# Kernel tuning notes

Measured on AMD Instinct MI355X. Metric: run time of the kernel, lower is better.

The kernel has to match this reference:

```python
import jax, jax.numpy as jnp
import numpy as np

N_NODES = 4096
N_EDGES = 16384
F_IN = 64
F_EDGE = 16
HID = 128
OUT = 64
N_GRAPHS = 32


def _encoder(x, edge_index, edge_attr, batch, p):
    N = x.shape[0]
    src, dst = edge_index[0], edge_index[1]
    # EdgeMLP: [E, F_edge] -> [E, F_in * HID] per-edge weight matrices
    h = jax.nn.relu(edge_attr @ p['e_w1'] + p['e_b1'])
    h = jax.nn.relu(h @ p['e_w2'] + p['e_b2'])
    Wmat = (h @ p['e_w3'] + p['e_b3']).reshape(-1, x.shape[1], p['root_w'].shape[1])  # [E, F_in, HID]
    # NNConv: message = x_src @ W_edge, scatter-add to dst, plus root transform + bias
    msg = jnp.einsum('ei,eio->eo', x[src], Wmat)  # [E, HID]
    agg = jax.ops.segment_sum(msg, dst, num_segments=N)
    h1 = jax.nn.relu(agg + x @ p['root_w'] + p['conv1_b'])  # [N, HID]
    # GATConv (1 head, concat=False) with self-loops (PyG default)
    loop = jnp.arange(N, dtype=src.dtype)
    si = jnp.concatenate([src, loop])
    di = jnp.concatenate([dst, loop])
    hp = h1 @ p['gat_w']  # [N, HID]
    a_s = hp @ p['att_src']  # [N]
    a_d = hp @ p['att_dst']  # [N]
    e = jax.nn.leaky_relu(a_s[si] + a_d[di], negative_slope=0.2)
    m = jax.ops.segment_max(e, di, num_segments=N)
    ex = jnp.exp(e - m[di])
    denom = jax.ops.segment_sum(ex, di, num_segments=N)
    alpha = ex / (denom[di] + 1e-16)
    h2 = jax.ops.segment_sum(alpha[:, None] * hp[si], di, num_segments=N) + p['gat_b']
    h2 = jax.nn.relu(h2)
    # global mean pool over graphs
    s = jax.ops.segment_sum(h2, batch, num_segments=N_GRAPHS)
    cnt = jax.ops.segment_sum(jnp.ones((N,), h2.dtype), batch, num_segments=N_GRAPHS)
    pooled = s / jnp.maximum(cnt, 1.0)[:, None]
    return jax.nn.relu(pooled @ p['fc1_w'] + p['fc1_b'])  # [B, OUT]


def setup_inputs() -> dict:
    key = jax.random.key(0)
    ks = jax.random.split(key, 24)
    d = {}
    d['x1'] = jax.random.normal(ks[0], (N_NODES, F_IN), jnp.float32)
    d['edge_index1'] = jax.random.randint(ks[1], (2, N_EDGES), 0, N_NODES)
    d['edge_attr1'] = jax.random.normal(ks[2], (N_EDGES, F_EDGE), jnp.float32)
    d['batch1'] = jnp.sort(jax.random.randint(ks[3], (N_NODES,), 0, N_GRAPHS))
    d['x2'] = jax.random.normal(ks[4], (N_NODES, F_IN), jnp.float32)
    d['edge_index2'] = jax.random.randint(ks[5], (2, N_EDGES), 0, N_NODES)
    d['edge_attr2'] = jax.random.normal(ks[6], (N_EDGES, F_EDGE), jnp.float32)
    d['batch2'] = jnp.sort(jax.random.randint(ks[7], (N_NODES,), 0, N_GRAPHS))

    def lin(k, fi, fo):
        return jax.random.normal(k, (fi, fo), jnp.float32) * (fi ** -0.5)

    d['e_w1'] = lin(ks[8], F_EDGE, 128); d['e_b1'] = jnp.zeros((128,), jnp.float32)
    d['e_w2'] = lin(ks[9], 128, 64); d['e_b2'] = jnp.zeros((64,), jnp.float32)
    d['e_w3'] = lin(ks[10], 64, F_IN * HID); d['e_b3'] = jnp.zeros((F_IN * HID,), jnp.float32)
    d['root_w'] = lin(ks[11], F_IN, HID); d['conv1_b'] = jnp.zeros((HID,), jnp.float32)
    d['gat_w'] = lin(ks[12], HID, HID)
    d['att_src'] = jax.random.normal(ks[13], (HID,), jnp.float32) * (HID ** -0.5)
    d['att_dst'] = jax.random.normal(ks[14], (HID,), jnp.float32) * (HID ** -0.5)
    d['gat_b'] = jnp.zeros((HID,), jnp.float32)
    d['fc1_w'] = lin(ks[15], HID, OUT); d['fc1_b'] = jnp.zeros((OUT,), jnp.float32)
    d['fc2_w'] = lin(ks[16], OUT, 1); d['fc2_b'] = jnp.zeros((1,), jnp.float32)
    return d


def reference(x1, edge_index1, edge_attr1, batch1, x2, edge_index2, edge_attr2, batch2,
              e_w1, e_b1, e_w2, e_b2, e_w3, e_b3, root_w, conv1_b,
              gat_w, att_src, att_dst, gat_b, fc1_w, fc1_b, fc2_w, fc2_b):
    p = dict(e_w1=e_w1, e_b1=e_b1, e_w2=e_w2, e_b2=e_b2, e_w3=e_w3, e_b3=e_b3,
             root_w=root_w, conv1_b=conv1_b, gat_w=gat_w, att_src=att_src,
             att_dst=att_dst, gat_b=gat_b, fc1_w=fc1_w, fc1_b=fc1_b,
             fc2_w=fc2_w, fc2_b=fc2_b)
    z1 = _encoder(x1, edge_index1, edge_attr1, batch1, p)
    z2 = _encoder(x2, edge_index2, edge_attr2, batch2, p)
    z = jnp.abs(z1 - z2) @ fc2_w + fc2_b  # [B, 1]
    return jax.nn.sigmoid(z).squeeze(1)  # [B]
```

## Files before the change

kernel.cpp:

```cpp
#include <hip/hip_runtime.h>
#include <hip/hip_bf16.h>
#include <math.h>

#define NN 4096
#define NE 16384
#define FIN 64
#define FE 16
#define HIDD 128
#define OUTD 64
#define NG 32
#define EP (NE + NN)
#define KSPLIT 2
#define NCH (64 / KSPLIT)

typedef __attribute__((ext_vector_type(4))) unsigned u4v;
typedef __attribute__((ext_vector_type(4))) float f4v;
typedef _Float16 f16x8 __attribute__((ext_vector_type(8)));

union FragH { u4v u; f16x8 h; };
union FH2 { _Float16 f[2]; unsigned u; };
union F16x8U { _Float16 f[8]; u4v u; };

#define PB_EMLP  4096
#define PB_BIAS  (PB_EMLP + 4096)
#define PB_HIST  (PB_BIAS + 32)
#define PB_TOTAL (PB_HIST + 64)

__global__ void k_prep(const float* __restrict__ ea0, const float* __restrict__ ea1,
                       const float* __restrict__ w1, const float* __restrict__ b1,
                       const float* __restrict__ w2, const float* __restrict__ b2,
                       const float* __restrict__ w3,
                       const float* __restrict__ X0, const float* __restrict__ X1,
                       const float* __restrict__ b3,
                       const int* __restrict__ ei0, const int* __restrict__ ei1,
                       unsigned short* __restrict__ B1t,
                       float* __restrict__ h0, float* __restrict__ h1g,
                       float* __restrict__ Bb0, float* __restrict__ Bb1,
                       int* __restrict__ rowcnt) {
    int b = blockIdx.x, t = threadIdx.x;
    if (b < PB_EMLP) {
        int gi = b >> 11;
        int e0 = (b & 2047) * 8;
        const float* ea = gi ? ea1 : ea0;
        float* hout = gi ? h1g : h0;
        __shared__ float h1s[8][HIDD];
#pragma unroll
        for (int r = 0; r < 4; ++r) {
            int idx = r * 256 + t;
            int e1 = idx >> 7, j = idx & 127;
            float acc = b1[j];
#pragma unroll
            for (int i = 0; i < FE; ++i) acc += ea[(e0 + e1) * FE + i] * w1[i * HIDD + j];
            h1s[e1][j] = fmaxf(acc, 0.f);
        }
        __syncthreads();
#pragma unroll
        for (int r = 0; r < 2; ++r) {
            int idx = r * 256 + t;
            int e1 = idx >> 6, j = idx & 63;
            float acc = b2[j];
#pragma unroll 16
            for (int k = 0; k < HIDD; ++k) acc += h1s[e1][k] * w2[k * 64 + j];
            hout[(size_t)(e0 + e1) * 64 + j] = fmaxf(acc, 0.f);
        }
    } else if (b < PB_BIAS) {
        int bb = b - PB_EMLP;
        int gi = bb >> 11;
        int n = (bb & 2047) * 2 + (t >> 7);
        int o = t & 127;
        const float* X = gi ? X1 : X0;
        float* Bb = gi ? Bb1 : Bb0;
        float acc = 0.f;
#pragma unroll 16
        for (int i = 0; i < FIN; ++i) acc += X[n * FIN + i] * b3[i * HIDD + o];
        Bb[(size_t)n * HIDD + o] = acc;
    } else if (b < PB_HIST) {
        int tid = (b - PB_BIAS) * 256 + t;
        for (int idx = tid; idx < 2 * EP; idx += 32 * 256) {
            int gi = idx / EP, e = idx % EP;
            const int* dst = (gi ? ei1 : ei0) + NE;
            int d = (e < NE) ? dst[e] : e - NE;
            atomicAdd(&rowcnt[gi * NN + d], 1);
        }
    } else {
        __shared__ float lds[64 * 129];
        int c = b - PB_HIST;
#pragma unroll
        for (int r = 0; r < 32; ++r) {
            int idx = r * 256 + t;
            lds[(idx >> 7) * 129 + (idx & 127)] = w3[(size_t)c * 8192 + idx];
        }
        __syncthreads();
#pragma unroll
        for (int r = 0; r < 32; ++r) {
            int e = r * 256 + t;
            float v = lds[(e & 63) * 129 + (e >> 6)];
            union { _Float16 f; unsigned short u; } cv;
            cv.f = (_Float16)v;
            B1t[(size_t)c * 8192 + e] = cv.u;
        }
    }
}

__global__ void k_scan(const int* __restrict__ rowcnt, int* __restrict__ rowptr,
                       const int* __restrict__ batch0, const int* __restrict__ batch1,
                       int* __restrict__ br) {
    int b = blockIdx.x;
    if (b < 2) {
        int gi = b;
        const int* cnt = rowcnt + gi * NN;
        int* rp = rowptr + gi * (NN + 1);
        int t = threadIdx.x;
        int lane = t & 63, w = t >> 6;
        int base = t * 4;
        int v0 = cnt[base], v1 = cnt[base + 1], v2 = cnt[base + 2], v3 = cnt[base + 3];
        int s = v0 + v1 + v2 + v3;
        int inc = s;
#pragma unroll
        for (int off = 1; off < 64; off <<= 1) {
            int u = __shfl_up(inc, off);
            if (lane >= off) inc += u;
        }
        __shared__ int wsum[16];
        if (lane == 63) wsum[w] = inc;
        __syncthreads();
        if (t < 16) {
            int ws = wsum[t];
            int wi = ws;
#pragma unroll
            for (int off = 1; off < 16; off <<= 1) {
                int u = __shfl_up(wi, off);
                if (t >= off) wi += u;
            }
            wsum[t] = wi - ws;
        }
        __syncthreads();
        int run = wsum[w] + inc - s;
        rp[base] = run; run += v0;
        rp[base + 1] = run; run += v1;
        rp[base + 2] = run; run += v2;
        rp[base + 3] = run; run += v3;
        if (t == 1023) rp[NN] = run;
    } else {
        int t = threadIdx.x;
        if (t < 66) {
            int gi = t / 33, g = t % 33;
            const int* batch = gi ? batch1 : batch0;
            int lo = 0, hi = NN;
            while (lo < hi) {
                int mid = (lo + hi) >> 1;
                if (batch[mid] < g) lo = mid + 1; else hi = mid;
            }
            br[gi * 33 + g] = lo;
        }
    }
}

__global__ void k_fill(const int* __restrict__ ei0, const int* __restrict__ ei1,
                       const int* __restrict__ rowptr, int* __restrict__ cnt2,
                       int* __restrict__ adj) {
    int idx = blockIdx.x * 256 + threadIdx.x;
    if (idx >= 2 * EP) return;
    int gi = idx / EP, e = idx % EP;
    const int* dst = (gi ? ei1 : ei0) + NE;
    int d = (e < NE) ? dst[e] : e - NE;
    int pos = rowptr[gi * (NN + 1) + d] + atomicAdd(&cnt2[gi * NN + d], 1);
    adj[gi * EP + pos] = e;
}

__global__ void __launch_bounds__(128, 2)
k_nnconv(const float* __restrict__ x0, const float* __restrict__ x1,
         const float* __restrict__ h_0, const float* __restrict__ h_1,
         const unsigned short* __restrict__ B1t,
         const float* __restrict__ Bb0, const float* __restrict__ Bb1,
         const int* __restrict__ ei0, const int* __restrict__ ei1,
         _Float16* __restrict__ msgh) {
    __shared__ __align__(16) float sm[32 * 128];
    int gi = blockIdx.z;
    const float* x = gi ? x1 : x0;
    const float* hh = gi ? h_1 : h_0;
    const float* Bb = gi ? Bb1 : Bb0;
    const int* src = gi ? ei1 : ei0;

    int t = threadIdx.x;
    int e0 = blockIdx.x * 64;
    int z = blockIdx.y;
    int ch = t >> 6;
    int l = t & 63, q4 = l >> 4, c16 = l & 15;

    FragH xf[4][2];
#pragma unroll
    for (int mf = 0; mf < 4; ++mf) {
        int s_ = src[e0 + mf * 16 + c16];
        const float* xr = &x[(size_t)s_ * FIN];
#pragma unroll
        for (int kf = 0; kf < 2; ++kf) {
            float xv[8];
            *(float4*)&xv[0] = *(const float4*)&xr[kf * 32 + q4 * 8];
            *(float4*)&xv[4] = *(const float4*)&xr[kf * 32 + q4 * 8 + 4];
            u4v w;
#pragma unroll
            for (int p = 0; p < 4; ++p) {
                FH2 c2;
                c2.f[0] = (_Float16)xv[2 * p];
                c2.f[1] = (_Float16)xv[2 * p + 1];
                w[p] = c2.u;
            }
            xf[mf][kf].u = w;
        }
    }

    f4v acc[4][4];
#pragma unroll
    for (int a = 0; a < 4; ++a)
#pragma unroll
        for (int b = 0; b < 4; ++b) acc[a][b] = (f4v){0.f, 0.f, 0.f, 0.f};

    const u4v* bp = (const u4v*)B1t;

#define LOADF(buf, cg)                                                          \
    {                                                                           \
        const u4v* cp = bp + (size_t)(cg) * 1024;                               \
        _Pragma("unroll") for (int kf = 0; kf < 2; ++kf)                        \
        _Pragma("unroll") for (int nf = 0; nf < 4; ++nf)                        \
            buf[kf * 4 + nf].u = cp[(ch * 64 + nf * 16 + c16) * 8 + kf * 4 + q4]; \
    }

#define DOMFMA(buf, COMP)                                                       \
    {                                                                           \
        __builtin_amdgcn_s_setprio(1);                                          \
        _Pragma("unroll") for (int mf = 0; mf < 4; ++mf) {                      \
            FH2 hp2;                                                            \
            hp2.f[0] = (_Float16)hv4[mf].COMP;                                  \
            hp2.f[1] = hp2.f[0];                                                \
            unsigned hw = hp2.u;                                                \
            FragH hb; hb.u = (u4v){hw, hw, hw, hw};                             \
            _Pragma("unroll") for (int kf = 0; kf < 2; ++kf) {                  \
                FragH a1;                                                       \
                a1.h = hb.h * xf[mf][kf].h;                                     \
                _Pragma("unroll") for (int nf = 0; nf < 4; ++nf) {              \
                    acc[mf][nf] = __builtin_amdgcn_mfma_f32_16x16x32_f16(       \
                        a1.h, buf[kf * 4 + nf].h, acc[mf][nf], 0, 0, 0);        \
                }                                                               \
            }                                                                   \
        }                                                                       \
        __builtin_amdgcn_s_setprio(0);                                          \
    }

    FragH bA[8], bB[8];
    float4 hv4[4];
    LOADF(bA, z * NCH);
#pragma unroll 1
    for (int cl = 0; cl < NCH; cl += 4) {
#pragma unroll
        for (int mf = 0; mf < 4; ++mf)
            hv4[mf] = *(const float4*)&hh[(size_t)(e0 + mf * 16 + c16) * 64 + z * NCH + cl];
        LOADF(bB, z * NCH + cl + 1);
        DOMFMA(bA, x);
        LOADF(bA, z * NCH + cl + 2);
        DOMFMA(bB, y);
        LOADF(bB, z * NCH + cl + 3);
        DOMFMA(bA, z);
        if (cl + 4 < NCH) LOADF(bA, z * NCH + cl + 4);
        DOMFMA(bB, w);
    }
#undef LOADF
#undef DOMFMA

    _Float16* mb = msgh + (size_t)(gi * KSPLIT + z) * NE * HIDD;
    int z0 = (z == 0);
#pragma unroll
    for (int half = 0; half < 2; ++half) {
        if (half) __syncthreads();
#pragma unroll
        for (int mf2 = 0; mf2 < 2; ++mf2) {
            int mf = half * 2 + mf2;
#pragma unroll
            for (int j = 0; j < 4; ++j) {
                int rr = mf2 * 16 + q4 * 4 + j;
#pragma unroll
                for (int nf = 0; nf < 4; ++nf)
                    sm[rr * 128 + ch * 64 + nf * 16 + c16] = acc[mf][nf][j];
            }
        }
        __syncthreads();
#pragma unroll
        for (int it = 0; it < 4; ++it) {
            int u = it * 128 + t;
            int row = u >> 4, c8 = u & 15;
            int eg = e0 + half * 32 + row;
            float v[8];
            *(float4*)&v[0] = *(float4*)&sm[row * 128 + c8 * 8];
            *(float4*)&v[4] = *(float4*)&sm[row * 128 + c8 * 8 + 4];
            if (z0) {
                int s_ = src[eg];
                const float* bbr = &Bb[(size_t)s_ * HIDD + c8 * 8];
#pragma unroll
                for (int j = 0; j < 8; ++j) v[j] += bbr[j];
            }
            F16x8U cv;
#pragma unroll
            for (int j = 0; j < 8; ++j) cv.f[j] = (_Float16)v[j];
            *(u4v*)&mb[(size_t)eg * HIDD + c8 * 8] = cv.u;
        }
    }
}

__global__ void k_h1hp(const _Float16* __restrict__ msgh,
                       const int* __restrict__ rowptr, const int* __restrict__ adj,
                       const float* __restrict__ X0, const float* __restrict__ X1,
                       const float* __restrict__ rw, const float* __restrict__ cb,
                       const float* __restrict__ gw,
                       const float* __restrict__ asw, const float* __restrict__ adw,
                       float* __restrict__ hp0, float* __restrict__ hp1,
                       float* __restrict__ a_s0, float* __restrict__ a_s1,
                       float* __restrict__ a_d0, float* __restrict__ a_d1) {
    int gi = blockIdx.y;
    const float* X = gi ? X1 : X0;
    float* hp = gi ? hp1 : hp0;
    float* a_s = gi ? a_s1 : a_s0;
    float* a_d = gi ? a_d1 : a_d0;
    const int* rp = rowptr + gi * (NN + 1);
    const int* aj = adj + gi * EP;
    const _Float16* m0 = msgh + (size_t)(gi * KSPLIT + 0) * NE * HIDD;
    const _Float16* m1 = msgh + (size_t)(gi * KSPLIT + 1) * NE * HIDD;
    int n0 = blockIdx.x * 16;
    int t = threadIdx.x;
    int o = t & 127, q = t >> 7;
    __shared__ float xsh[16][FIN];
    __shared__ float h1s[16][HIDD];
    __shared__ float s1[16][2], s2[16][2];
#pragma unroll
    for (int r = 0; r < 2; ++r) {
        int idx = r * 512 + t;
        xsh[idx >> 6][idx & 63] = X[(n0 + (idx >> 6)) * FIN + (idx & 63)];
    }
    __syncthreads();
    float accs[4];
#pragma unroll
    for (int nn = 0; nn < 4; ++nn) {
        int n = n0 + q * 4 + nn;
        float acc = cb[o];
        int lo = rp[n], hi = rp[n + 1];
        for (int p = lo; p < hi; ++p) {
            int e = aj[p];
            if (e < NE) {
                size_t eo = (size_t)e * HIDD + o;
                acc += (float)m0[eo] + (float)m1[eo];
            }
        }
        accs[nn] = acc;
    }
#pragma unroll 8
    for (int i = 0; i < FIN; ++i) {
        float w = rw[i * HIDD + o];
#pragma unroll
        for (int nn = 0; nn < 4; ++nn) accs[nn] += xsh[q * 4 + nn][i] * w;
    }
#pragma unroll
    for (int nn = 0; nn < 4; ++nn) h1s[q * 4 + nn][o] = fmaxf(accs[nn], 0.f);
    __syncthreads();
#pragma unroll
    for (int nn = 0; nn < 4; ++nn) accs[nn] = 0.f;
#pragma unroll 8
    for (int k = 0; k < HIDD; ++k) {
        float w = gw[k * HIDD + o];
#pragma unroll
        for (int nn = 0; nn < 4; ++nn) accs[nn] += h1s[q * 4 + nn][k] * w;
    }
#pragma unroll
    for (int nn = 0; nn < 4; ++nn) {
        int n = n0 + q * 4 + nn;
        hp[(size_t)n * HIDD + o] = accs[nn];
        float p1 = accs[nn] * asw[o], p2 = accs[nn] * adw[o];
#pragma unroll
        for (int off = 32; off; off >>= 1) {
            p1 += __shfl_down(p1, off);
            p2 += __shfl_down(p2, off);
        }
        if ((o & 63) == 0) { s1[q * 4 + nn][o >> 6] = p1; s2[q * 4 + nn][o >> 6] = p2; }
    }
    __syncthreads();
    if (t < 16) {
        a_s[n0 + t] = s1[t][0] + s1[t][1];
        a_d[n0 + t] = s2[t][0] + s2[t][1];
    }
}

__global__ void k_gat(const int* __restrict__ rowptr, const int* __restrict__ adj,
                      const int* __restrict__ ei0, const int* __restrict__ ei1,
                      const float* __restrict__ hp0, const float* __restrict__ hp1,
                      const float* __restrict__ as0, const float* __restrict__ as1,
                      const float* __restrict__ ad0, const float* __restrict__ ad1,
                      const float* __restrict__ gb,
                      float* __restrict__ h2_0, float* __restrict__ h2_1) {
    int gi = blockIdx.y;
    const int* src = gi ? ei1 : ei0;
    const float* hp = gi ? hp1 : hp0;
    const float* a_s = gi ? as1 : as0;
    const float* a_d = gi ? ad1 : ad0;
    float* h2 = gi ? h2_1 : h2_0;
    const int* rp = rowptr + gi * (NN + 1);
    const int* aj = adj + gi * EP;
    int w = threadIdx.x >> 6, l = threadIdx.x & 63;
    int n = blockIdx.x * 4 + w;
    int lo = rp[n], deg = rp[n + 1] - lo;
    float adn = a_d[n];
    float m = -1e30f;
    for (int base = 0; base < deg; base += 64) {
        float sc = -1e30f;
        int j = base + l;
        if (j < deg) {
            int e = aj[lo + j];
            int si = (e < NE) ? src[e] : n;
            float xsc = a_s[si] + adn;
            sc = xsc > 0.f ? xsc : 0.2f * xsc;
        }
#pragma unroll
        for (int off = 32; off; off >>= 1) sc = fmaxf(sc, __shfl_xor(sc, off));
        m = fmaxf(m, sc);
    }
    float den = 0.f;
    for (int base = 0; base < deg; base += 64) {
        float ev = 0.f;
        int j = base + l;
        if (j < deg) {
            int e = aj[lo + j];
            int si = (e < NE) ? src[e] : n;
            float xsc = a_s[si] + adn;
            float sc = xsc > 0.f ? xsc : 0.2f * xsc;
            ev = expf(sc - m);
        }
#pragma unroll
        for (int off = 32; off; off >>= 1) ev += __shfl_xor(ev, off);
        den += ev;
    }
    float inv = 1.f / (den + 1e-16f);
    float acc0 = 0.f, acc1 = 0.f;
    for (int j = 0; j < deg; ++j) {
        int e = aj[lo + j];
        int si = (e < NE) ? src[e] : n;
        float xsc = a_s[si] + adn;
        float sc = xsc > 0.f ? xsc : 0.2f * xsc;
        float al = expf(sc - m) * inv;
        acc0 += al * hp[(size_t)si * HIDD + l];
        acc1 += al * hp[(size_t)si * HIDD + 64 + l];
    }
    h2[(size_t)n * HIDD + l] = fmaxf(acc0 + gb[l], 0.f);
    h2[(size_t)n * HIDD + 64 + l] = fmaxf(acc1 + gb[64 + l], 0.f);
}

__global__ void k_poolfc1(const float* __restrict__ h2_0, const float* __restrict__ h2_1,
                          const int* __restrict__ br,
                          const float* __restrict__ w, const float* __restrict__ bias,
                          float* __restrict__ z) {
    int gi = blockIdx.x >> 5, g = blockIdx.x & 31;
    const float* h2 = gi ? h2_1 : h2_0;
    int lo = br[gi * 33 + g], hi = br[gi * 33 + g + 1];
    int t = threadIdx.x;
    __shared__ float pool[HIDD];
    float acc = 0.f;
    for (int n = lo; n < hi; ++n) acc += h2[(size_t)n * HIDD + t];
    pool[t] = acc;
    __syncthreads();
    if (t < 64) {
        float c = fmaxf((float)(hi - lo), 1.f);
        float a = bias[t];
#pragma unroll 16
        for (int o = 0; o < HIDD; ++o) a += (pool[o] / c) * w[o * OUTD + t];
        z[gi * NG * OUTD + g * OUTD + t] = fmaxf(a, 0.f);
    }
}

__global__ void k_final(const float* __restrict__ zz,
                        const float* __restrict__ w, const float* __restrict__ b,
                        float* __restrict__ out) {
    int g = threadIdx.x;
    const float* z1 = zz;
    const float* z2 = zz + NG * OUTD;
    float acc = b[0];
#pragma unroll
    for (int j = 0; j < OUTD; ++j) acc += fabsf(z1[g * OUTD + j] - z2[g * OUTD + j]) * w[j];
    out[g] = 1.f / (1.f + expf(-acc));
}

extern "C" void kernel_launch(void* const* d_in, const int* in_sizes, int n_in,
                              void* d_out, int out_size, void* d_ws, size_t ws_size,
                              hipStream_t stream) {
    const float* x0     = (const float*)d_in[0];
    const int*   ei0    = (const int*)d_in[1];
    const float* ea0    = (const float*)d_in[2];
    const int*   b0     = (const int*)d_in[3];
    const float* x1     = (const float*)d_in[4];
    const int*   ei1    = (const int*)d_in[5];
    const float* ea1    = (const float*)d_in[6];
    const int*   b1     = (const int*)d_in[7];
    const float* e_w1 = (const float*)d_in[8];
    const float* e_b1 = (const float*)d_in[9];
    const float* e_w2 = (const float*)d_in[10];
    const float* e_b2 = (const float*)d_in[11];
    const float* e_w3 = (const float*)d_in[12];
    const float* e_b3 = (const float*)d_in[13];
    const float* root_w = (const float*)d_in[14];
    const float* conv1_b = (const float*)d_in[15];
    const float* gat_w = (const float*)d_in[16];
    const float* att_src = (const float*)d_in[17];
    const float* att_dst = (const float*)d_in[18];
    const float* gat_b = (const float*)d_in[19];
    const float* fc1_w = (const float*)d_in[20];
    const float* fc1_b = (const float*)d_in[21];
    const float* fc2_w = (const float*)d_in[22];
    const float* fc2_b = (const float*)d_in[23];

    float* ws = (float*)d_ws;
    size_t off = 0;
    auto alloc = [&](size_t n) { float* p = ws + off; off += n; return p; };
    int* rowcnt = (int*)alloc(2 * NN);
    int* cnt2   = (int*)alloc(2 * NN);
    size_t zero_elems = off;
    int* rowptr = (int*)alloc(2 * (NN + 1));
    int* br     = (int*)alloc(66);
    int* adj    = (int*)alloc(2 * EP);
    float* h[2]   = {alloc((size_t)NE * 64), alloc((size_t)NE * 64)};
    unsigned short* B1t = (unsigned short*)alloc((size_t)4096 * 128 / 2);
    float* Bb[2]  = {alloc((size_t)NN * HIDD), alloc((size_t)NN * HIDD)};
    _Float16* msgh = (_Float16*)alloc((size_t)2 * KSPLIT * NE * HIDD / 2);
    float* hp[2]  = {alloc((size_t)NN * HIDD), alloc((size_t)NN * HIDD)};
    float* a_s[2] = {alloc(NN), alloc(NN)};
    float* a_d[2] = {alloc(NN), alloc(NN)};
    float* h2[2]  = {alloc((size_t)NN * HIDD), alloc((size_t)NN * HIDD)};
    float* zz     = alloc((size_t)2 * NG * OUTD);

    (void)hipMemsetAsync(ws, 0, zero_elems * 4, stream);
    k_prep<<<PB_TOTAL, 256, 0, stream>>>(ea0, ea1, e_w1, e_b1, e_w2, e_b2, e_w3,
                                         x0, x1, e_b3, ei0, ei1,
                                         B1t, h[0], h[1], Bb[0], Bb[1],
                                         rowcnt);
    k_scan<<<3, 1024, 0, stream>>>(rowcnt, rowptr, b0, b1, br);
    k_fill<<<(2 * EP + 255) / 256, 256, 0, stream>>>(ei0, ei1, rowptr, cnt2, adj);
    k_nnconv<<<dim3(NE / 64, KSPLIT, 2), 128, 0, stream>>>(
        x0, x1, h[0], h[1], B1t, Bb[0], Bb[1], ei0, ei1, msgh);
    k_h1hp<<<dim3(NN / 16, 2), 512, 0, stream>>>(
        msgh, rowptr, adj, x0, x1, root_w, conv1_b, gat_w, att_src, att_dst,
        hp[0], hp[1], a_s[0], a_s[1], a_d[0], a_d[1]);
    k_gat<<<dim3(NN / 4, 2), 256, 0, stream>>>(
        rowptr, adj, ei0, ei1, hp[0], hp[1], a_s[0], a_s[1], a_d[0], a_d[1],
        gat_b, h2[0], h2[1]);
    k_poolfc1<<<64, HIDD, 0, stream>>>(h2[0], h2[1], br, fc1_w, fc1_b, zz);
    k_final<<<1, NG, 0, stream>>>(zz, fc2_w, fc2_b, (float*)d_out);
}
```

Measured before the change: 239.9 us.

## Enlarge per-block tiles in edge MLP and h1hp, fuse final head into pool

```diff
diff --git a/kernel.cpp b/kernel.cpp
--- a/kernel.cpp
+++ b/kernel.cpp
@@ -21,7 +21,7 @@
 union FH2 { _Float16 f[2]; unsigned u; };
 union F16x8U { _Float16 f[8]; u4v u; };
 
-#define PB_EMLP  4096
+#define PB_EMLP  1024
 #define PB_BIAS  (PB_EMLP + 4096)
 #define PB_HIST  (PB_BIAS + 32)
 #define PB_TOTAL (PB_HIST + 64)
@@ -39,13 +39,13 @@
                        int* __restrict__ rowcnt) {
     int b = blockIdx.x, t = threadIdx.x;
     if (b < PB_EMLP) {
-        int gi = b >> 11;
-        int e0 = (b & 2047) * 8;
+        int gi = b >> 9;
+        int e0 = (b & 511) * 32;
         const float* ea = gi ? ea1 : ea0;
         float* hout = gi ? h1g : h0;
-        __shared__ float h1s[8][HIDD];
-#pragma unroll
-        for (int r = 0; r < 4; ++r) {
+        __shared__ float h1s[32][HIDD];
+#pragma unroll
+        for (int r = 0; r < 16; ++r) {
             int idx = r * 256 + t;
             int e1 = idx >> 7, j = idx & 127;
             float acc = b1[j];
@@ -55,7 +55,7 @@
         }
         __syncthreads();
 #pragma unroll
-        for (int r = 0; r < 2; ++r) {
+        for (int r = 0; r < 8; ++r) {
             int idx = r * 256 + t;
             int e1 = idx >> 6, j = idx & 63;
             float acc = b2[j];
@@ -324,22 +324,22 @@
     const int* aj = adj + gi * EP;
     const _Float16* m0 = msgh + (size_t)(gi * KSPLIT + 0) * NE * HIDD;
     const _Float16* m1 = msgh + (size_t)(gi * KSPLIT + 1) * NE * HIDD;
-    int n0 = blockIdx.x * 16;
+    int n0 = blockIdx.x * 32;
     int t = threadIdx.x;
     int o = t & 127, q = t >> 7;
-    __shared__ float xsh[16][FIN];
-    __shared__ float h1s[16][HIDD];
-    __shared__ float s1[16][2], s2[16][2];
-#pragma unroll
-    for (int r = 0; r < 2; ++r) {
+    __shared__ float xsh[32][FIN];
+    __shared__ float h1s[32][HIDD];
+    __shared__ float s1[32][2], s2[32][2];
+#pragma unroll
+    for (int r = 0; r < 4; ++r) {
         int idx = r * 512 + t;
         xsh[idx >> 6][idx & 63] = X[(n0 + (idx >> 6)) * FIN + (idx & 63)];
     }
     __syncthreads();
-    float accs[4];
-#pragma unroll
-    for (int nn = 0; nn < 4; ++nn) {
-        int n = n0 + q * 4 + nn;
+    float accs[8];
+#pragma unroll
+    for (int nn = 0; nn < 8; ++nn) {
+        int n = n0 + q * 8 + nn;
         float acc = cb[o];
         int lo = rp[n], hi = rp[n + 1];
         for (int p = lo; p < hi; ++p) {
@@ -355,22 +355,22 @@
     for (int i = 0; i < FIN; ++i) {
         float w = rw[i * HIDD + o];
 #pragma unroll
-        for (int nn = 0; nn < 4; ++nn) accs[nn] += xsh[q * 4 + nn][i] * w;
-    }
-#pragma unroll
-    for (int nn = 0; nn < 4; ++nn) h1s[q * 4 + nn][o] = fmaxf(accs[nn], 0.f);
+        for (int nn = 0; nn < 8; ++nn) accs[nn] += xsh[q * 8 + nn][i] * w;
+    }
+#pragma unroll
+    for (int nn = 0; nn < 8; ++nn) h1s[q * 8 + nn][o] = fmaxf(accs[nn], 0.f);
     __syncthreads();
 #pragma unroll
-    for (int nn = 0; nn < 4; ++nn) accs[nn] = 0.f;
+    for (int nn = 0; nn < 8; ++nn) accs[nn] = 0.f;
 #pragma unroll 8
     for (int k = 0; k < HIDD; ++k) {
         float w = gw[k * HIDD + o];
 #pragma unroll
-        for (int nn = 0; nn < 4; ++nn) accs[nn] += h1s[q * 4 + nn][k] * w;
-    }
-#pragma unroll
-    for (int nn = 0; nn < 4; ++nn) {
-        int n = n0 + q * 4 + nn;
+        for (int nn = 0; nn < 8; ++nn) accs[nn] += h1s[q * 8 + nn][k] * w;
+    }
+#pragma unroll
+    for (int nn = 0; nn < 8; ++nn) {
+        int n = n0 + q * 8 + nn;
         hp[(size_t)n * HIDD + o] = accs[nn];
         float p1 = accs[nn] * asw[o], p2 = accs[nn] * adw[o];
 #pragma unroll
@@ -378,10 +378,10 @@
             p1 += __shfl_down(p1, off);
             p2 += __shfl_down(p2, off);
         }
-        if ((o & 63) == 0) { s1[q * 4 + nn][o >> 6] = p1; s2[q * 4 + nn][o >> 6] = p2; }
+        if ((o & 63) == 0) { s1[q * 8 + nn][o >> 6] = p1; s2[q * 8 + nn][o >> 6] = p2; }
     }
     __syncthreads();
-    if (t < 16) {
+    if (t < 32) {
         a_s[n0 + t] = s1[t][0] + s1[t][1];
         a_d[n0 + t] = s2[t][0] + s2[t][1];
     }
@@ -453,7 +453,9 @@
 __global__ void k_poolfc1(const float* __restrict__ h2_0, const float* __restrict__ h2_1,
                           const int* __restrict__ br,
                           const float* __restrict__ w, const float* __restrict__ bias,
-                          float* __restrict__ z) {
+                          const float* __restrict__ fc2w, const float* __restrict__ fc2b,
+                          float* __restrict__ z, unsigned* __restrict__ done,
+                          float* __restrict__ out) {
     int gi = blockIdx.x >> 5, g = blockIdx.x & 31;
     const float* h2 = gi ? h2_1 : h2_0;
     int lo = br[gi * 33 + g], hi = br[gi * 33 + g + 1];
@@ -470,18 +472,22 @@
         for (int o = 0; o < HIDD; ++o) a += (pool[o] / c) * w[o * OUTD + t];
         z[gi * NG * OUTD + g * OUTD + t] = fmaxf(a, 0.f);
     }
-}
-
-__global__ void k_final(const float* __restrict__ zz,
-                        const float* __restrict__ w, const float* __restrict__ b,
-                        float* __restrict__ out) {
-    int g = threadIdx.x;
-    const float* z1 = zz;
-    const float* z2 = zz + NG * OUTD;
-    float acc = b[0];
-#pragma unroll
-    for (int j = 0; j < OUTD; ++j) acc += fabsf(z1[g * OUTD + j] - z2[g * OUTD + j]) * w[j];
-    out[g] = 1.f / (1.f + expf(-acc));
+    __syncthreads();
+    __threadfence();
+    __shared__ unsigned rank;
+    if (t == 0) rank = atomicAdd(done, 1u);
+    __syncthreads();
+    if (rank == 63) {
+        __threadfence();
+        const volatile float* zv = z;
+        if (t < NG) {
+            float a = fc2b[0];
+#pragma unroll
+            for (int j = 0; j < OUTD; ++j)
+                a += fabsf(zv[t * OUTD + j] - zv[NG * OUTD + t * OUTD + j]) * fc2w[j];
+            out[t] = 1.f / (1.f + expf(-a));
+        }
+    }
 }
 
 extern "C" void kernel_launch(void* const* d_in, const int* in_sizes, int n_in,
@@ -517,6 +523,7 @@
     auto alloc = [&](size_t n) { float* p = ws + off; off += n; return p; };
     int* rowcnt = (int*)alloc(2 * NN);
     int* cnt2   = (int*)alloc(2 * NN);
+    unsigned* done = (unsigned*)alloc(1);
     size_t zero_elems = off;
     int* rowptr = (int*)alloc(2 * (NN + 1));
     int* br     = (int*)alloc(66);
@@ -540,12 +547,12 @@
     k_fill<<<(2 * EP + 255) / 256, 256, 0, stream>>>(ei0, ei1, rowptr, cnt2, adj);
     k_nnconv<<<dim3(NE / 64, KSPLIT, 2), 128, 0, stream>>>(
         x0, x1, h[0], h[1], B1t, Bb[0], Bb[1], ei0, ei1, msgh);
-    k_h1hp<<<dim3(NN / 16, 2), 512, 0, stream>>>(
+    k_h1hp<<<dim3(NN / 32, 2), 512, 0, stream>>>(
         msgh, rowptr, adj, x0, x1, root_w, conv1_b, gat_w, att_src, att_dst,
         hp[0], hp[1], a_s[0], a_s[1], a_d[0], a_d[1]);
     k_gat<<<dim3(NN / 4, 2), 256, 0, stream>>>(
         rowptr, adj, ei0, ei1, hp[0], hp[1], a_s[0], a_s[1], a_d[0], a_d[1],
         gat_b, h2[0], h2[1]);
-    k_poolfc1<<<64, HIDD, 0, stream>>>(h2[0], h2[1], br, fc1_w, fc1_b, zz);
-    k_final<<<1, NG, 0, stream>>>(zz, fc2_w, fc2_b, (float*)d_out);
-}
+    k_poolfc1<<<64, HIDD, 0, stream>>>(h2[0], h2[1], br, fc1_w, fc1_b,
+                                       fc2_w, fc2_b, zz, done, (float*)d_out);
+}
```

New measurement: 271.6 us. 13.2% more time.
